# Performance work log

Hardware: AMD Instinct MI355X
Metric: run time of the kernel (lower is better)

The kernel has to match this reference:

```python
import jax, jax.numpy as jnp
import numpy as np

B, S, H = 32, 2048, 1024

def setup_inputs() -> dict:
    key = jax.random.key(0)
    ks = jax.random.split(key, 6)
    sc = 1.0 / np.sqrt(H)  # keep projections well-scaled
    return {
        "decoder_hidden_state": jax.random.normal(ks[0], (B, H), jnp.float32),
        "encoder_outputs": jax.random.normal(ks[1], (B, S, H), jnp.float32),
        "Wq": jax.random.normal(ks[2], (H, H), jnp.float32) * sc,
        "bq": jnp.zeros((H,), jnp.float32),
        "Wk": jax.random.normal(ks[3], (H, H), jnp.float32) * sc,
        "bk": jnp.zeros((H,), jnp.float32),
        "Wv": jax.random.normal(ks[4], (H, H), jnp.float32) * sc,
        "bv": jnp.zeros((H,), jnp.float32),
        "alpha": jnp.full((1,), 0.5, jnp.float32),  # DyT scalar alpha
        "gamma": jnp.ones((H,), jnp.float32),
        "beta": jnp.zeros((H,), jnp.float32),
    }


def reference(decoder_hidden_state, encoder_outputs, Wq, bq, Wk, bk, Wv, bv, alpha, gamma, beta):
    # projections (torch Linear: x @ W.T + b)
    q = decoder_hidden_state @ Wq.T + bq            # [B, H]
    k = jnp.einsum("bsh,oh->bso", encoder_outputs, Wk) + bk  # [B, S, H]
    v = jnp.einsum("bsh,oh->bso", encoder_outputs, Wv) + bv  # [B, S, H]
    d_k = q.shape[-1]
    energy = jnp.einsum("bh,bsh->bs", q, k) / jnp.sqrt(jnp.asarray(d_k, q.dtype))
    attention_weights = jax.nn.softmax(energy, axis=1)       # [B, S]
    context = jnp.einsum("bs,bsh->bh", attention_weights, v)  # [B, H]
    # DyT norm: gamma * tanh(alpha * x) + beta
    context = gamma * jnp.tanh(alpha * context) + beta
    return (context, attention_weights)
```

## Files before the change

### kernel.cpp

```cpp
#include <hip/hip_runtime.h>

#define B 32
#define S 2048
#define HDIM 1024
#define INV_SQRT_H 0.03125f

#define WS_Q    0
#define WS_QB   (32*1024)
#define WS_QWP  (WS_QB + 64)
#define WS_E    (WS_QWP + 4*32*1024)
#define WS_L    (WS_E + B*S)
#define WS_ACC  (WS_L + 32*64)
#define WS_C    (WS_ACC + 32*64*1024)

__device__ __forceinline__ float dot4(float4 a, float4 b) {
    return a.x*b.x + a.y*b.y + a.z*b.z + a.w*b.w;
}

__device__ __forceinline__ float wave_reduce_add(float v) {
#pragma unroll
    for (int off = 32; off >= 1; off >>= 1) v += __shfl_xor(v, off);
    return v;
}

__global__ __launch_bounds__(256) void k_q(const float* __restrict__ dec,
                                           const float* __restrict__ Wq,
                                           const float* __restrict__ bq,
                                           float* __restrict__ ws) {
    int bg = blockIdx.x >> 7;
    int oc = blockIdx.x & 127;
    int wave = threadIdx.x >> 6, lane = threadIdx.x & 63;
    int b0 = bg * 4;
    const float4* D = (const float4*)dec;
    float4 dv[4][4];
#pragma unroll
    for (int bb = 0; bb < 4; ++bb)
#pragma unroll
        for (int c = 0; c < 4; ++c)
            dv[bb][c] = D[(size_t)(b0 + bb) * 256 + c * 64 + lane];
#pragma unroll
    for (int i = 0; i < 2; ++i) {
        int o = oc * 8 + wave * 2 + i;
        const float4* w4 = (const float4*)(Wq + (size_t)o * HDIM);
        float4 a0 = w4[lane], a1 = w4[64+lane], a2 = w4[128+lane], a3 = w4[192+lane];
        float bqo = bq[o];
#pragma unroll
        for (int bb = 0; bb < 4; ++bb) {
            float d = dot4(a0, dv[bb][0]) + dot4(a1, dv[bb][1])
                    + dot4(a2, dv[bb][2]) + dot4(a3, dv[bb][3]);
            d = wave_reduce_add(d);
            if (lane == 0) ws[WS_Q + (b0 + bb) * HDIM + o] = d + bqo;
        }
    }
}

__global__ __launch_bounds__(256) void k_qw(const float* __restrict__ Wk,
                                            const float* __restrict__ bk,
                                            float* __restrict__ ws) {
    __shared__ float lds[4][64];
    int b  = blockIdx.x >> 6;
    int hc = (blockIdx.x >> 2) & 15;
    int qc = blockIdx.x & 3;
    int t = threadIdx.x;
    int col = hc * 64 + (t & 63);
    int os = t >> 6;
    const float* q = ws + WS_Q + b * HDIM;
    int o0 = qc * 256 + os * 64;
    float acc = 0.f;
#pragma unroll 4
    for (int o = o0; o < o0 + 64; ++o)
        acc += q[o] * Wk[(size_t)o * HDIM + col];
    lds[os][t & 63] = acc;
    __syncthreads();
    if (t < 64)
        ws[WS_QWP + (size_t)(qc * 32 + b) * HDIM + hc * 64 + t]
            = lds[0][t] + lds[1][t] + lds[2][t] + lds[3][t];
    if (hc == 0 && qc == 0 && t < 64) {
        const float4* q4 = (const float4*)q;
        const float4* bk4 = (const float4*)bk;
        float s2 = 0.f;
#pragma unroll
        for (int c = 0; c < 4; ++c) s2 += dot4(q4[64*c + t], bk4[64*c + t]);
        s2 = wave_reduce_add(s2);
        if (t == 0) ws[WS_QB + b] = s2 * INV_SQRT_H;
    }
}

__global__ __launch_bounds__(256, 6) void k_flash(const float* __restrict__ enc,
                                                  float* __restrict__ ws) {
    __shared__ float lacc[4][HDIM];
    __shared__ float ll[4];
    int b = blockIdx.x >> 6;
    int ch = blockIdx.x & 63;
    int wave = threadIdx.x >> 6, lane = threadIdx.x & 63;

    const float4* P4 = (const float4*)(ws + WS_QWP);
    float4 w0, w1, w2, w3;
    {
        float4 t0 = P4[(size_t)(0*32 + b) * 256 +   0 + lane];
        float4 t1 = P4[(size_t)(1*32 + b) * 256 +   0 + lane];
        float4 t2 = P4[(size_t)(2*32 + b) * 256 +   0 + lane];
        float4 t3 = P4[(size_t)(3*32 + b) * 256 +   0 + lane];
        w0 = make_float4(t0.x+t1.x+t2.x+t3.x, t0.y+t1.y+t2.y+t3.y,
                         t0.z+t1.z+t2.z+t3.z, t0.w+t1.w+t2.w+t3.w);
        t0 = P4[(size_t)(0*32 + b) * 256 +  64 + lane];
        t1 = P4[(size_t)(1*32 + b) * 256 +  64 + lane];
        t2 = P4[(size_t)(2*32 + b) * 256 +  64 + lane];
        t3 = P4[(size_t)(3*32 + b) * 256 +  64 + lane];
        w1 = make_float4(t0.x+t1.x+t2.x+t3.x, t0.y+t1.y+t2.y+t3.y,
                         t0.z+t1.z+t2.z+t3.z, t0.w+t1.w+t2.w+t3.w);
        t0 = P4[(size_t)(0*32 + b) * 256 + 128 + lane];
        t1 = P4[(size_t)(1*32 + b) * 256 + 128 + lane];
        t2 = P4[(size_t)(2*32 + b) * 256 + 128 + lane];
        t3 = P4[(size_t)(3*32 + b) * 256 + 128 + lane];
        w2 = make_float4(t0.x+t1.x+t2.x+t3.x, t0.y+t1.y+t2.y+t3.y,
                         t0.z+t1.z+t2.z+t3.z, t0.w+t1.w+t2.w+t3.w);
        t0 = P4[(size_t)(0*32 + b) * 256 + 192 + lane];
        t1 = P4[(size_t)(1*32 + b) * 256 + 192 + lane];
        t2 = P4[(size_t)(2*32 + b) * 256 + 192 + lane];
        t3 = P4[(size_t)(3*32 + b) * 256 + 192 + lane];
        w3 = make_float4(t0.x+t1.x+t2.x+t3.x, t0.y+t1.y+t2.y+t3.y,
                         t0.z+t1.z+t2.z+t3.z, t0.w+t1.w+t2.w+t3.w);
    }
    float qbs = ws[WS_QB + b];

    float l_run = 0.f;
    float4 A0 = {0,0,0,0}, A1 = A0, A2 = A0, A3 = A0;

    int s0 = ch * 32 + wave * 8;
    const float4* R = (const float4*)enc + (size_t)(b * S + s0) * 256;

#pragma unroll 2
    for (int i = 0; i < 8; ++i) {
        const float4* Ri = R + (size_t)i * 256;
        float4 e0 = Ri[lane], e1 = Ri[64+lane], e2 = Ri[128+lane], e3 = Ri[192+lane];
        float d = dot4(e0,w0) + dot4(e1,w1) + dot4(e2,w2) + dot4(e3,w3);
        d = wave_reduce_add(d);
        float p = __expf(d * INV_SQRT_H + qbs);
        if (lane == 0) ws[WS_E + b * S + s0 + i] = p;
        l_run += p;
        A0.x += p*e0.x; A0.y += p*e0.y; A0.z += p*e0.z; A0.w += p*e0.w;
        A1.x += p*e1.x; A1.y += p*e1.y; A1.z += p*e1.z; A1.w += p*e1.w;
        A2.x += p*e2.x; A2.y += p*e2.y; A2.z += p*e2.z; A2.w += p*e2.w;
        A3.x += p*e3.x; A3.y += p*e3.y; A3.z += p*e3.z; A3.w += p*e3.w;
    }

    float4* la4 = (float4*)lacc[wave];
    la4[lane] = A0; la4[64+lane] = A1; la4[128+lane] = A2; la4[192+lane] = A3;
    if (lane == 0) ll[wave] = l_run;
    __syncthreads();

    int t = threadIdx.x;
    float4 c0 = ((float4*)lacc[0])[t];
    float4 c1 = ((float4*)lacc[1])[t];
    float4 c2 = ((float4*)lacc[2])[t];
    float4 c3 = ((float4*)lacc[3])[t];
    float4 cc;
    cc.x = c0.x + c1.x + c2.x + c3.x;
    cc.y = c0.y + c1.y + c2.y + c3.y;
    cc.z = c0.z + c1.z + c2.z + c3.z;
    cc.w = c0.w + c1.w + c2.w + c3.w;
    ((float4*)(ws + WS_ACC))[(size_t)(b * 64 + ch) * 256 + t] = cc;
    if (t == 0) ws[WS_L + b * 64 + ch] = ll[0] + ll[1] + ll[2] + ll[3];
}

__global__ __launch_bounds__(256) void k_combine(float* __restrict__ ws,
                                                 float* __restrict__ out) {
    __shared__ float s_inv;
    int t = threadIdx.x;
    if (blockIdx.x < 32) {
        int b = blockIdx.x;
        if (t < 64) {
            float li = ws[WS_L + b * 64 + t];
            float lg = wave_reduce_add(li);
            if (t == 0) s_inv = 1.f / lg;
        }
        __syncthreads();
        float inv_lg = s_inv;
        const float4* acc4 = ((const float4*)(ws + WS_ACC)) + (size_t)b * 64 * 256;
        float4 c = {0, 0, 0, 0};
#pragma unroll 4
        for (int i = 0; i < 64; ++i) {
            float4 a = acc4[(size_t)i * 256 + t];
            c.x += a.x; c.y += a.y; c.z += a.z; c.w += a.w;
        }
        c.x *= inv_lg; c.y *= inv_lg; c.z *= inv_lg; c.w *= inv_lg;
        ((float4*)(ws + WS_C))[b * 256 + t] = c;
    } else {
        int gt = (blockIdx.x - 32) * 256 + t;
        int b = gt >> 11;
        if (t < 64) {
            float li = ws[WS_L + b * 64 + t];
            float lg = wave_reduce_add(li);
            if (t == 0) s_inv = 1.f / lg;
        }
        __syncthreads();
        out[B * HDIM + gt] = ws[WS_E + gt] * s_inv;
    }
}

__global__ __launch_bounds__(256) void k_out(const float* __restrict__ Wv,
                                             const float* __restrict__ bv,
                                             const float* __restrict__ alpha,
                                             const float* __restrict__ gamma,
                                             const float* __restrict__ beta,
                                             const float* __restrict__ ws,
                                             float* __restrict__ out) {
    int bg = blockIdx.x >> 7;
    int oc = blockIdx.x & 127;
    int wave = threadIdx.x >> 6, lane = threadIdx.x & 63;
    int b0 = bg * 4;
    const float4* C4 = (const float4*)(ws + WS_C);
    float4 dv[4][4];
#pragma unroll
    for (int bb = 0; bb < 4; ++bb)
#pragma unroll
        for (int c = 0; c < 4; ++c)
            dv[bb][c] = C4[(size_t)(b0 + bb) * 256 + c * 64 + lane];
    float al = alpha[0];
#pragma unroll
    for (int i = 0; i < 2; ++i) {
        int o = oc * 8 + wave * 2 + i;
        const float4* w4 = (const float4*)(Wv + (size_t)o * HDIM);
        float4 a0 = w4[lane], a1 = w4[64+lane], a2 = w4[128+lane], a3 = w4[192+lane];
        float bvo = bv[o], gm = gamma[o], bt = beta[o];
#pragma unroll
        for (int bb = 0; bb < 4; ++bb) {
            float d = dot4(a0, dv[bb][0]) + dot4(a1, dv[bb][1])
                    + dot4(a2, dv[bb][2]) + dot4(a3, dv[bb][3]);
            d = wave_reduce_add(d);
            if (lane == 0) {
                float y = d + bvo;
                out[(b0 + bb) * HDIM + o] = gm * tanhf(al * y) + bt;
            }
        }
    }
}

extern "C" void kernel_launch(void* const* d_in, const int* in_sizes, int n_in,
                              void* d_out, int out_size, void* d_ws, size_t ws_size,
                              hipStream_t stream) {
    const float* dec   = (const float*)d_in[0];
    const float* enc   = (const float*)d_in[1];
    const float* Wq    = (const float*)d_in[2];
    const float* bq    = (const float*)d_in[3];
    const float* Wk    = (const float*)d_in[4];
    const float* bk    = (const float*)d_in[5];
    const float* Wv    = (const float*)d_in[6];
    const float* bv    = (const float*)d_in[7];
    const float* alpha = (const float*)d_in[8];
    const float* gamma = (const float*)d_in[9];
    const float* beta  = (const float*)d_in[10];
    float* out = (float*)d_out;
    float* ws  = (float*)d_ws;

    hipLaunchKernelGGL(k_q,       dim3(1024), dim3(256), 0, stream, dec, Wq, bq, ws);
    hipLaunchKernelGGL(k_qw,      dim3(2048), dim3(256), 0, stream, Wk, bk, ws);
    hipLaunchKernelGGL(k_flash,   dim3(2048), dim3(256), 0, stream, enc, ws);
    hipLaunchKernelGGL(k_combine, dim3(288),  dim3(256), 0, stream, ws, out);
    hipLaunchKernelGGL(k_out,     dim3(1024), dim3(256), 0, stream, Wv, bv, alpha, gamma, beta, ws, out);
}
```

Baseline: 81.36 us.

## Replace split-K partial buffers with atomic accumulation and merge combine into output kernel

The flash kernel now atomically adds its per-chunk context sums and softmax denominators into small zero-initialized buffers (zeroed in k_qw) instead of writing 64 partials per batch to workspace. The separate combine kernel is removed: normalization of attention weights and of the context is folded into a single final kernel that also does the Wv projection and DyT. This removes a launch and an 8 MB partial write/read round trip, at the cost of float atomic contention and nondeterministic summation order.

```diff
diff --git a/kernel.cpp b/kernel.cpp
--- a/kernel.cpp
+++ b/kernel.cpp
@@ -9,9 +9,8 @@
 #define WS_QB   (32*1024)
 #define WS_QWP  (WS_QB + 64)
 #define WS_E    (WS_QWP + 4*32*1024)
-#define WS_L    (WS_E + B*S)
-#define WS_ACC  (WS_L + 32*64)
-#define WS_C    (WS_ACC + 32*64*1024)
+#define WS_CHAT (WS_E + B*S)
+#define WS_LG   (WS_CHAT + 32*1024)
 
 __device__ __forceinline__ float dot4(float4 a, float4 b) {
     return a.x*b.x + a.y*b.y + a.z*b.z + a.w*b.w;
@@ -75,14 +74,18 @@
     if (t < 64)
         ws[WS_QWP + (size_t)(qc * 32 + b) * HDIM + hc * 64 + t]
             = lds[0][t] + lds[1][t] + lds[2][t] + lds[3][t];
-    if (hc == 0 && qc == 0 && t < 64) {
-        const float4* q4 = (const float4*)q;
-        const float4* bk4 = (const float4*)bk;
-        float s2 = 0.f;
-#pragma unroll
-        for (int c = 0; c < 4; ++c) s2 += dot4(q4[64*c + t], bk4[64*c + t]);
-        s2 = wave_reduce_add(s2);
-        if (t == 0) ws[WS_QB + b] = s2 * INV_SQRT_H;
+    if (hc == 0 && qc == 0) {
+        ((float4*)(ws + WS_CHAT))[b * 256 + t] = make_float4(0.f, 0.f, 0.f, 0.f);
+        if (t == 65) ws[WS_LG + b] = 0.f;
+        if (t < 64) {
+            const float4* q4 = (const float4*)q;
+            const float4* bk4 = (const float4*)bk;
+            float s2 = 0.f;
+#pragma unroll
+            for (int c = 0; c < 4; ++c) s2 += dot4(q4[64*c + t], bk4[64*c + t]);
+            s2 = wave_reduce_add(s2);
+            if (t == 0) ws[WS_QB + b] = s2 * INV_SQRT_H;
+        }
     }
 }
 
@@ -160,63 +163,44 @@
     cc.y = c0.y + c1.y + c2.y + c3.y;
     cc.z = c0.z + c1.z + c2.z + c3.z;
     cc.w = c0.w + c1.w + c2.w + c3.w;
-    ((float4*)(ws + WS_ACC))[(size_t)(b * 64 + ch) * 256 + t] = cc;
-    if (t == 0) ws[WS_L + b * 64 + ch] = ll[0] + ll[1] + ll[2] + ll[3];
-}
-
-__global__ __launch_bounds__(256) void k_combine(float* __restrict__ ws,
-                                                 float* __restrict__ out) {
-    __shared__ float s_inv;
+    float* CH = ws + WS_CHAT + b * HDIM + t * 4;
+    atomicAdd(CH + 0, cc.x);
+    atomicAdd(CH + 1, cc.y);
+    atomicAdd(CH + 2, cc.z);
+    atomicAdd(CH + 3, cc.w);
+    if (t == 0) atomicAdd(ws + WS_LG + b, ll[0] + ll[1] + ll[2] + ll[3]);
+}
+
+__global__ __launch_bounds__(256) void k_final(const float* __restrict__ Wv,
+                                               const float* __restrict__ bv,
+                                               const float* __restrict__ alpha,
+                                               const float* __restrict__ gamma,
+                                               const float* __restrict__ beta,
+                                               const float* __restrict__ ws,
+                                               float* __restrict__ out) {
     int t = threadIdx.x;
-    if (blockIdx.x < 32) {
-        int b = blockIdx.x;
-        if (t < 64) {
-            float li = ws[WS_L + b * 64 + t];
-            float lg = wave_reduce_add(li);
-            if (t == 0) s_inv = 1.f / lg;
-        }
-        __syncthreads();
-        float inv_lg = s_inv;
-        const float4* acc4 = ((const float4*)(ws + WS_ACC)) + (size_t)b * 64 * 256;
-        float4 c = {0, 0, 0, 0};
-#pragma unroll 4
-        for (int i = 0; i < 64; ++i) {
-            float4 a = acc4[(size_t)i * 256 + t];
-            c.x += a.x; c.y += a.y; c.z += a.z; c.w += a.w;
-        }
-        c.x *= inv_lg; c.y *= inv_lg; c.z *= inv_lg; c.w *= inv_lg;
-        ((float4*)(ws + WS_C))[b * 256 + t] = c;
-    } else {
-        int gt = (blockIdx.x - 32) * 256 + t;
+    if (blockIdx.x < 256) {
+        int gt = blockIdx.x * 256 + t;
         int b = gt >> 11;
-        if (t < 64) {
-            float li = ws[WS_L + b * 64 + t];
-            float lg = wave_reduce_add(li);
-            if (t == 0) s_inv = 1.f / lg;
-        }
-        __syncthreads();
-        out[B * HDIM + gt] = ws[WS_E + gt] * s_inv;
-    }
-}
-
-__global__ __launch_bounds__(256) void k_out(const float* __restrict__ Wv,
-                                             const float* __restrict__ bv,
-                                             const float* __restrict__ alpha,
-                                             const float* __restrict__ gamma,
-                                             const float* __restrict__ beta,
-                                             const float* __restrict__ ws,
-                                             float* __restrict__ out) {
-    int bg = blockIdx.x >> 7;
-    int oc = blockIdx.x & 127;
-    int wave = threadIdx.x >> 6, lane = threadIdx.x & 63;
+        float inv = 1.f / ws[WS_LG + b];
+        out[B * HDIM + gt] = ws[WS_E + gt] * inv;
+        return;
+    }
+    int blk = blockIdx.x - 256;
+    int bg = blk >> 7;
+    int oc = blk & 127;
+    int wave = t >> 6, lane = t & 63;
     int b0 = bg * 4;
-    const float4* C4 = (const float4*)(ws + WS_C);
+    const float4* C4 = (const float4*)(ws + WS_CHAT);
     float4 dv[4][4];
-#pragma unroll
-    for (int bb = 0; bb < 4; ++bb)
+    float invl[4];
+#pragma unroll
+    for (int bb = 0; bb < 4; ++bb) {
+        invl[bb] = 1.f / ws[WS_LG + b0 + bb];
 #pragma unroll
         for (int c = 0; c < 4; ++c)
             dv[bb][c] = C4[(size_t)(b0 + bb) * 256 + c * 64 + lane];
+    }
     float al = alpha[0];
 #pragma unroll
     for (int i = 0; i < 2; ++i) {
@@ -230,7 +214,7 @@
                     + dot4(a2, dv[bb][2]) + dot4(a3, dv[bb][3]);
             d = wave_reduce_add(d);
             if (lane == 0) {
-                float y = d + bvo;
+                float y = d * invl[bb] + bvo;
                 out[(b0 + bb) * HDIM + o] = gm * tanhf(al * y) + bt;
             }
         }
@@ -254,9 +238,8 @@
     float* out = (float*)d_out;
     float* ws  = (float*)d_ws;
 
-    hipLaunchKernelGGL(k_q,       dim3(1024), dim3(256), 0, stream, dec, Wq, bq, ws);
-    hipLaunchKernelGGL(k_qw,      dim3(2048), dim3(256), 0, stream, Wk, bk, ws);
-    hipLaunchKernelGGL(k_flash,   dim3(2048), dim3(256), 0, stream, enc, ws);
-    hipLaunchKernelGGL(k_combine, dim3(288),  dim3(256), 0, stream, ws, out);
-    hipLaunchKernelGGL(k_out,     dim3(1024), dim3(256), 0, stream, Wv, bv, alpha, gamma, beta, ws, out);
-}
+    hipLaunchKernelGGL(k_q,     dim3(1024), dim3(256), 0, stream, dec, Wq, bq, ws);
+    hipLaunchKernelGGL(k_qw,    dim3(2048), dim3(256), 0, stream, Wk, bk, ws);
+    hipLaunchKernelGGL(k_flash, dim3(2048), dim3(256), 0, stream, enc, ws);
+    hipLaunchKernelGGL(k_final, dim3(1280), dim3(256), 0, stream, Wv, bv, alpha, gamma, beta, ws, out);
+}
```

Result: slower. 91.37 us (+12.3%).
